# Kernel optimization log

Hardware: AMD Instinct MI355X
Metric: run time of the kernel (lower is better)

The kernel has to match this reference:

```python
import jax, jax.numpy as jnp
import numpy as np

B, M, E, NPOS, F, NHEAD, NLAYERS, DFF = 32, 512, 512, 1024, 768, 8, 2, 2048
S = M + 1

def _pe(embed, pad):
    pos = np.arange(pad, dtype=np.float32)[:, None]
    i = np.arange(embed)[None, :]
    ang = pos / np.power(10000.0, (i // 2 * 2.0) / embed)
    pe = np.where(i % 2 == 0, np.sin(ang), np.cos(ang))
    return jnp.asarray(pe, jnp.float32)

PE = _pe(E, M)  # [M, E] sinusoidal table, matches pos_embedding()

def _ln(x, w, b, eps=1e-5):
    mu = x.mean(-1, keepdims=True)
    var = ((x - mu) ** 2).mean(-1, keepdims=True)
    return (x - mu) / jnp.sqrt(var + eps) * w + b

def _mha(x, wi, bi, wo, bo):
    # x: [L, N, E] where L is the attended axis (torch seq dim)
    L, N, Em = x.shape
    Dh = Em // NHEAD
    q, k, v = jnp.split(x @ wi.T + bi, 3, axis=-1)
    q = q.reshape(L, N, NHEAD, Dh) * np.float32(1.0 / np.sqrt(Dh))
    k = k.reshape(L, N, NHEAD, Dh)
    v = v.reshape(L, N, NHEAD, Dh)
    att = jax.nn.softmax(jnp.einsum('lnhd,mnhd->nhlm', q, k), axis=-1)
    o = jnp.einsum('nhlm,mnhd->lnhd', att, v).reshape(L, N, Em)
    return o @ wo.T + bo

def _encoder(x, enc):
    wi, bi, wo, bo, ln1w, ln1b, ln2w, ln2b, w1, b1, w2, b2 = enc
    for l in range(NLAYERS):  # post-norm TransformerEncoderLayer, ReLU, eval mode
        x = _ln(x + _mha(x, wi[l], bi[l], wo[l], bo[l]), ln1w[l], ln1b[l])
        h = jax.nn.relu(x @ w1[l].T + b1[l]) @ w2[l].T + b2[l]
        x = _ln(x + h, ln2w[l], ln2b[l])
    return x

def _forward(pos1, pos2, bert_feature, final_base, emb_table, enc, w_model, w_disc, b_disc):
    emb_table = emb_table.at[0].set(0.0)  # padding_idx=0
    embed = emb_table[pos2] + PE          # [B, M, E]
    starts, ends = pos1[..., 0], pos1[..., 1]
    # loop breaks at first span with end==0: valid = prefix of nonzero ends
    valid = jnp.cumprod((ends != 0).astype(jnp.int32), axis=1).astype(bool)
    k = jnp.arange(M)
    cover = valid[:, :, None] & (starts[:, :, None] <= k) & (k < ends[:, :, None])  # [B, Mspan, Mpos]
    # later spans overwrite earlier ones -> take max covering span index
    span_id = jnp.max(jnp.where(cover, jnp.arange(M)[None, :, None], -1), axis=1)  # [B, Mpos]
    filled = jnp.take_along_axis(embed, jnp.clip(span_id, 0, M - 1)[..., None], axis=1)
    final = jnp.where(span_id[..., None] >= 0, filled, final_base)  # [B, M, E]
    cls = jnp.broadcast_to(emb_table[1], (B, 1, E))
    x = jnp.concatenate([cls, final], axis=1)  # [B, S, E]; torch encoder treats dim0 as seq
    x = _encoder(x, enc)
    pos_feature = jnp.tanh(x @ w_model.T)      # [B, S, F]
    z = jnp.concatenate([bert_feature, pos_feature], axis=-1) @ w_disc.T + b_disc
    return jax.nn.sigmoid(z)                   # [B, S, 1]

def setup_inputs():
    key = jax.random.key(0)
    ks = jax.random.split(key, 12)
    sc = 0.02
    n_valid, chunk = 120, 4  # contiguous spans [4j, 4j+4) for j < 120, then end==0 terminator
    j = np.arange(M)
    starts = np.where(j < n_valid, j * chunk, 0)
    ends = np.where(j < n_valid, j * chunk + chunk, 0)
    pos1 = np.broadcast_to(np.stack([starts, ends], -1), (B, M, 2)).astype(np.int32)
    return {
        'pos1': jnp.asarray(pos1),
        'pos2': jax.random.randint(ks[0], (B, M), 2, NPOS),
        'bert_feature': jax.random.normal(ks[1], (B, S, F), jnp.float32),
        'final_base': jax.random.uniform(ks[2], (B, M, E), jnp.float32),
        'emb_table': jax.random.normal(ks[3], (NPOS, E), jnp.float32) * sc,
        'enc_in_proj_w': jax.random.normal(ks[4], (NLAYERS, 3 * E, E), jnp.float32) * sc,
        'enc_in_proj_b': jnp.zeros((NLAYERS, 3 * E), jnp.float32),
        'enc_out_proj_w': jax.random.normal(ks[5], (NLAYERS, E, E), jnp.float32) * sc,
        'enc_out_proj_b': jnp.zeros((NLAYERS, E), jnp.float32),
        'enc_ln1_w': jnp.ones((NLAYERS, E), jnp.float32),
        'enc_ln1_b': jnp.zeros((NLAYERS, E), jnp.float32),
        'enc_ln2_w': jnp.ones((NLAYERS, E), jnp.float32),
        'enc_ln2_b': jnp.zeros((NLAYERS, E), jnp.float32),
        'enc_ffn_w1': jax.random.normal(ks[6], (NLAYERS, DFF, E), jnp.float32) * sc,
        'enc_ffn_b1': jnp.zeros((NLAYERS, DFF), jnp.float32),
        'enc_ffn_w2': jax.random.normal(ks[7], (NLAYERS, E, DFF), jnp.float32) * sc,
        'enc_ffn_b2': jnp.zeros((NLAYERS, E), jnp.float32),
        'w_model': jax.random.normal(ks[8], (F, E), jnp.float32) * sc,
        'w_disc': jax.random.normal(ks[9], (1, 2 * F), jnp.float32) * sc,
        'b_disc': jnp.zeros((1,), jnp.float32),
    }

def reference(pos1, pos2, bert_feature, final_base, emb_table,
              enc_in_proj_w, enc_in_proj_b, enc_out_proj_w, enc_out_proj_b,
              enc_ln1_w, enc_ln1_b, enc_ln2_w, enc_ln2_b,
              enc_ffn_w1, enc_ffn_b1, enc_ffn_w2, enc_ffn_b2,
              w_model, w_disc, b_disc):
    enc = (enc_in_proj_w, enc_in_proj_b, enc_out_proj_w, enc_out_proj_b,
           enc_ln1_w, enc_ln1_b, enc_ln2_w, enc_ln2_b,
           enc_ffn_w1, enc_ffn_b1, enc_ffn_w2, enc_ffn_b2)
    return _forward(pos1, pos2, bert_feature, final_base, emb_table, enc, w_model, w_disc, b_disc)
```

## Files before the change

### kernel.cpp

```cpp
#include <hip/hip_runtime.h>
#include <hip/hip_bf16.h>

#define B_   32
#define M_   512
#define E_   512
#define S_   513
#define T_   (B_ * S_)
#define TP_  16512
#define NH_  8
#define DH_  64
#define F_   768
#define DFF_ 2048

#define GMT_ 129

typedef short short8 __attribute__((ext_vector_type(8)));
typedef float floatx4 __attribute__((ext_vector_type(4)));

__device__ __forceinline__ float bf2f(unsigned short u) {
    return __uint_as_float(((unsigned int)u) << 16);
}
__device__ __forceinline__ unsigned short f2b_rne(float f) {
    unsigned int u = __float_as_uint(f);
    unsigned int r = u + 0x7FFF + ((u >> 16) & 1);
    return (unsigned short)(r >> 16);
}
__device__ __forceinline__ void gload16(const void* g, void* l) {
    __builtin_amdgcn_global_load_lds(
        (const __attribute__((address_space(1))) void*)g,
        (__attribute__((address_space(3))) void*)l, 16, 0, 0);
}

__global__ void span_kernel(const int* __restrict__ pos1, int* __restrict__ span) {
    int b = blockIdx.x;
    __shared__ int st[M_], en[M_];
    __shared__ int redm[4];
    int tid = threadIdx.x;
    for (int j = tid; j < M_; j += 256) {
        st[j] = pos1[(b * M_ + j) * 2];
        en[j] = pos1[(b * M_ + j) * 2 + 1];
    }
    __syncthreads();
    int idx = M_;
    for (int j = tid; j < M_; j += 256)
        if (en[j] == 0 && j < idx) idx = j;
    for (int off = 32; off; off >>= 1) idx = min(idx, __shfl_down(idx, off));
    if ((tid & 63) == 0) redm[tid >> 6] = idx;
    __syncthreads();
    int n = min(min(redm[0], redm[1]), min(redm[2], redm[3]));
    for (int k = tid; k < M_; k += 256) {
        int best = -1;
        for (int j = 0; j < n; ++j)
            if (st[j] <= k && k < en[j]) best = j;
        span[b * M_ + k] = best;
    }
}

__global__ void f2b5_kernel(const float* __restrict__ s0, const float* __restrict__ s1,
                            const float* __restrict__ s2, const float* __restrict__ s3,
                            const float* __restrict__ s4,
                            unsigned short* __restrict__ dst,
                            int c0, int c1, int c2, int c3, int c4) {
    int i = (blockIdx.x * 256 + threadIdx.x) * 4;
    if (i >= c4) return;
    const float* src;
    if      (i < c0) src = s0 + i;
    else if (i < c1) src = s1 + (i - c0);
    else if (i < c2) src = s2 + (i - c1);
    else if (i < c3) src = s3 + (i - c2);
    else             src = s4 + (i - c3);
    float4 v = *(const float4*)src;
    ushort4 o;
    o.x = f2b_rne(v.x); o.y = f2b_rne(v.y); o.z = f2b_rne(v.z); o.w = f2b_rne(v.w);
    *(ushort4*)&dst[i] = o;
}

__global__ __launch_bounds__(256) void build_x(const float* __restrict__ emb,
                        const int* __restrict__ pos2,
                        const float* __restrict__ fbase,
                        const int* __restrict__ span,
                        float* __restrict__ x,
                        unsigned short* __restrict__ xb) {
    int gid = blockIdx.x * 256 + threadIdx.x;
    int t  = gid >> 6;
    int e0 = (gid & 63) * 8;
    int s = t % S_;
    int b = t / S_;
    float v[8];
    if (s == 0) {
        float4 a = *(const float4*)&emb[E_ + e0];
        float4 c = *(const float4*)&emb[E_ + e0 + 4];
        v[0]=a.x; v[1]=a.y; v[2]=a.z; v[3]=a.w; v[4]=c.x; v[5]=c.y; v[6]=c.z; v[7]=c.w;
    } else {
        int k = s - 1;
        int sid = span[b * M_ + k];
        if (sid >= 0) {
            int p = pos2[b * M_ + sid];
            const float* er = emb + (size_t)p * E_ + e0;
            float4 a = *(const float4*)er;
            float4 c = *(const float4*)(er + 4);
            v[0]=a.x; v[1]=a.y; v[2]=a.z; v[3]=a.w; v[4]=c.x; v[5]=c.y; v[6]=c.z; v[7]=c.w;
            float fs = (float)sid;
#pragma unroll
            for (int jj = 0; jj < 4; ++jj) {
                float ex = (float)(e0 + 2 * jj) * (1.0f / 512.0f);
                float ang = fs * exp2f(-ex * 13.287712379549449f);
                float sn, cs;
                __sincosf(ang, &sn, &cs);
                v[2 * jj]     += sn;
                v[2 * jj + 1] += cs;
            }
        } else {
            const float* fr = fbase + ((size_t)b * M_ + k) * E_ + e0;
            float4 a = *(const float4*)fr;
            float4 c = *(const float4*)(fr + 4);
            v[0]=a.x; v[1]=a.y; v[2]=a.z; v[3]=a.w; v[4]=c.x; v[5]=c.y; v[6]=c.z; v[7]=c.w;
        }
    }
    size_t o = (size_t)t * E_ + e0;
    *(float4*)&x[o]     = make_float4(v[0], v[1], v[2], v[3]);
    *(float4*)&x[o + 4] = make_float4(v[4], v[5], v[6], v[7]);
    short8 ob;
#pragma unroll
    for (int j = 0; j < 8; ++j) ob[j] = (short)f2b_rne(v[j]);
    *(short8*)&xb[o] = ob;
}

template <int ACT, int KT>
__global__ __launch_bounds__(256, 3) void gemm_bf16(const unsigned short* __restrict__ A,
                                                    const unsigned short* __restrict__ W,
                                                    const float* __restrict__ bias,
                                                    unsigned short* __restrict__ Cb,
                                                    int T, int O,
                                                    const float* __restrict__ wdz,
                                                    float* __restrict__ zout) {
    constexpr int K = KT;
    constexpr int NSTEP = K / 32;
    __shared__ __align__(16) unsigned short sA[3][128 * 32];
    __shared__ __align__(16) unsigned short sB[3][128 * 32];
    int tid = threadIdx.x;
    int lane = tid & 63, wv = tid >> 6;
    int wr = (wv >> 1) * 64, wc = (wv & 1) * 64;

    int gn = O / 128;
    int per_panel = 8 * gn;
    int id = blockIdx.x;
    int p = id / per_panel;
    int r = id - p * per_panel;
    int mrem = GMT_ - p * 8; if (mrem > 8) mrem = 8;
    int mt = p * 8 + r % mrem;
    int nt = r / mrem;
    int t0 = mt * 128, o0 = nt * 128;

    floatx4 acc[4][4] = {};

    int swz_st = (((lane & 3) ^ ((lane >> 3) & 3))) * 8;
    const unsigned short* Ag = A + (size_t)(t0 + wv * 32 + (lane >> 2)) * K + swz_st;
    const unsigned short* Bg = W + (size_t)(o0 + wv * 32 + (lane >> 2)) * K + swz_st;
    const size_t row16 = (size_t)16 * K;
    const int wvo = wv * 1024;

    int fr = lane & 15;
    int fks = (((lane >> 4) ^ ((lane >> 1) & 3))) * 8;

    auto stage = [&](unsigned short* da, unsigned short* db, int k) {
        gload16(Ag + k, da + wvo);
        gload16(Ag + row16 + k, da + wvo + 512);
        gload16(Bg + k, db + wvo);
        gload16(Bg + row16 + k, db + wvo + 512);
    };
    auto compute = [&](const unsigned short* ca, const unsigned short* cb) {
        short8 af[4], bfr[4];
#pragma unroll
        for (int i = 0; i < 4; ++i)
            af[i] = *(const short8*)&ca[(wr + i * 16 + fr) * 32 + fks];
#pragma unroll
        for (int j = 0; j < 4; ++j)
            bfr[j] = *(const short8*)&cb[(wc + j * 16 + fr) * 32 + fks];
        __builtin_amdgcn_s_setprio(1);
#pragma unroll
        for (int i = 0; i < 4; ++i)
#pragma unroll
            for (int j = 0; j < 4; ++j)
                acc[i][j] = __builtin_amdgcn_mfma_f32_16x16x32_bf16(af[i], bfr[j], acc[i][j], 0, 0, 0);
        __builtin_amdgcn_s_setprio(0);
    };

    unsigned short *a0 = sA[0], *a1 = sA[1], *a2 = sA[2];
    unsigned short *b0 = sB[0], *b1 = sB[1], *b2 = sB[2];

    stage(a0, b0, 0);
    stage(a1, b1, 32);

#pragma unroll 3
    for (int t = 0; t < NSTEP - 2; ++t) {
        asm volatile("s_waitcnt vmcnt(4)" ::: "memory");
        __builtin_amdgcn_s_barrier();
        asm volatile("" ::: "memory");
        stage(a2, b2, (t + 2) * 32);
        compute(a0, b0);
        unsigned short* ta = a0; a0 = a1; a1 = a2; a2 = ta;
        unsigned short* tb = b0; b0 = b1; b1 = b2; b2 = tb;
    }
    asm volatile("s_waitcnt vmcnt(4)" ::: "memory");
    __builtin_amdgcn_s_barrier();
    asm volatile("" ::: "memory");
    compute(a0, b0);
    a0 = a1; b0 = b1;
    asm volatile("s_waitcnt vmcnt(0)" ::: "memory");
    __builtin_amdgcn_s_barrier();
    asm volatile("" ::: "memory");
    compute(a0, b0);

    int cr = (lane >> 4) * 4;
    int cc = lane & 15;
    if (ACT == 2) {
        float zp[4][4];
#pragma unroll
        for (int i = 0; i < 4; ++i)
#pragma unroll
            for (int rr = 0; rr < 4; ++rr) zp[i][rr] = 0.f;
#pragma unroll
        for (int j = 0; j < 4; ++j) {
            int gn_ = o0 + wc + j * 16 + cc;
            float wz = wdz[gn_];
#pragma unroll
            for (int i = 0; i < 4; ++i)
#pragma unroll
                for (int rr = 0; rr < 4; ++rr)
                    zp[i][rr] += tanhf(acc[i][j][rr]) * wz;
        }
#pragma unroll
        for (int i = 0; i < 4; ++i)
#pragma unroll
            for (int rr = 0; rr < 4; ++rr) {
                float v = zp[i][rr];
                v += __shfl_xor(v, 1);
                v += __shfl_xor(v, 2);
                v += __shfl_xor(v, 4);
                v += __shfl_xor(v, 8);
                if (cc == 0) {
                    int gm_ = t0 + wr + i * 16 + cr + rr;
                    if (gm_ < T) atomicAdd(&zout[gm_], v);
                }
            }
        return;
    }
#pragma unroll
    for (int i = 0; i < 4; ++i) {
#pragma unroll
        for (int j = 0; j < 4; ++j) {
            int gn_ = o0 + wc + j * 16 + cc;
            float bv = bias ? bias[gn_] : 0.f;
#pragma unroll
            for (int rr = 0; rr < 4; ++rr) {
                int gm_ = t0 + wr + i * 16 + cr + rr;
                if (gm_ >= T) continue;
                float v = acc[i][j][rr] + bv;
                if (ACT == 1) v = fmaxf(v, 0.f);
                Cb[(size_t)gm_ * O + gn_] = f2b_rne(v);
            }
        }
    }
}

__global__ __launch_bounds__(64) void attn_mfma(const unsigned short* __restrict__ qkv,
                                                unsigned short* __restrict__ o) {
    __shared__ __align__(16) unsigned short vt[64 * 40];
    __shared__ __align__(16) unsigned short ps[32 * 40];
    int s = blockIdx.x, h = blockIdx.y;
    int lane = threadIdx.x;
    int hd = h * 64;
    int fr = lane & 15, fq = lane >> 4;

    {
        int m = lane >> 1;
        int d0 = (lane & 1) * 32;
        const unsigned short* vrow = qkv + ((size_t)m * S_ + s) * 1536 + 1024 + hd + d0;
        short8 v0 = *(const short8*)(vrow);
        short8 v1 = *(const short8*)(vrow + 8);
        short8 v2 = *(const short8*)(vrow + 16);
        short8 v3 = *(const short8*)(vrow + 24);
#pragma unroll
        for (int j = 0; j < 8; ++j) {
            vt[(d0 + j) * 40 + m]      = (unsigned short)v0[j];
            vt[(d0 + 8 + j) * 40 + m]  = (unsigned short)v1[j];
            vt[(d0 + 16 + j) * 40 + m] = (unsigned short)v2[j];
            vt[(d0 + 24 + j) * 40 + m] = (unsigned short)v3[j];
        }
    }

    floatx4 c[2][2] = {};
#pragma unroll
    for (int ks = 0; ks < 2; ++ks) {
        short8 aq[2], bk[2];
#pragma unroll
        for (int lt = 0; lt < 2; ++lt) {
            int l = lt * 16 + fr;
            aq[lt] = *(const short8*)(qkv + ((size_t)l * S_ + s) * 1536 + hd + ks * 32 + fq * 8);
        }
#pragma unroll
        for (int mt = 0; mt < 2; ++mt) {
            int m = mt * 16 + fr;
            bk[mt] = *(const short8*)(qkv + ((size_t)m * S_ + s) * 1536 + 512 + hd + ks * 32 + fq * 8);
        }
#pragma unroll
        for (int lt = 0; lt < 2; ++lt)
#pragma unroll
            for (int mt = 0; mt < 2; ++mt)
                c[lt][mt] = __builtin_amdgcn_mfma_f32_16x16x32_bf16(aq[lt], bk[mt], c[lt][mt], 0, 0, 0);
    }

#pragma unroll
    for (int lt = 0; lt < 2; ++lt) {
#pragma unroll
        for (int r = 0; r < 4; ++r) {
            float a = c[lt][0][r] * 0.125f;
            float b = c[lt][1][r] * 0.125f;
            float mx = fmaxf(a, b);
#pragma unroll
            for (int off = 1; off < 16; off <<= 1) mx = fmaxf(mx, __shfl_xor(mx, off));
            float ea = expf(a - mx), eb = expf(b - mx);
            float sm = ea + eb;
#pragma unroll
            for (int off = 1; off < 16; off <<= 1) sm += __shfl_xor(sm, off);
            float inv = 1.f / sm;
            int l = lt * 16 + fq * 4 + r;
            ps[l * 40 + fr]      = f2b_rne(ea * inv);
            ps[l * 40 + 16 + fr] = f2b_rne(eb * inv);
        }
    }
    __syncthreads();

    short8 pa[2], vb[4];
#pragma unroll
    for (int lt = 0; lt < 2; ++lt)
        pa[lt] = *(const short8*)&ps[(lt * 16 + fr) * 40 + fq * 8];
#pragma unroll
    for (int dt = 0; dt < 4; ++dt)
        vb[dt] = *(const short8*)&vt[(dt * 16 + fr) * 40 + fq * 8];

    floatx4 oa[2][4] = {};
#pragma unroll
    for (int lt = 0; lt < 2; ++lt)
#pragma unroll
        for (int dt = 0; dt < 4; ++dt)
            oa[lt][dt] = __builtin_amdgcn_mfma_f32_16x16x32_bf16(pa[lt], vb[dt], oa[lt][dt], 0, 0, 0);

#pragma unroll
    for (int lt = 0; lt < 2; ++lt)
#pragma unroll
        for (int dt = 0; dt < 4; ++dt)
#pragma unroll
            for (int r = 0; r < 4; ++r) {
                int l = lt * 16 + fq * 4 + r;
                o[((size_t)l * S_ + s) * E_ + hd + dt * 16 + fr] = f2b_rne(oa[lt][dt][r]);
            }
}

__global__ __launch_bounds__(256) void add_ln(float* __restrict__ x,
                                              unsigned short* __restrict__ xb,
                                              const unsigned short* __restrict__ h,
                                              const float* __restrict__ w,
                                              const float* __restrict__ b) {
    int t = (blockIdx.x << 2) + (threadIdx.x >> 6);
    int lane = threadIdx.x & 63;
    int i0 = lane * 8;
    float* xr = x + (size_t)t * E_;
    const unsigned short* hr = h + (size_t)t * E_;
    float4 xv0 = *(const float4*)&xr[i0];
    float4 xv1 = *(const float4*)&xr[i0 + 4];
    short8 hv = *(const short8*)&hr[i0];
    float v[8];
    v[0] = xv0.x + bf2f((unsigned short)hv[0]);
    v[1] = xv0.y + bf2f((unsigned short)hv[1]);
    v[2] = xv0.z + bf2f((unsigned short)hv[2]);
    v[3] = xv0.w + bf2f((unsigned short)hv[3]);
    v[4] = xv1.x + bf2f((unsigned short)hv[4]);
    v[5] = xv1.y + bf2f((unsigned short)hv[5]);
    v[6] = xv1.z + bf2f((unsigned short)hv[6]);
    v[7] = xv1.w + bf2f((unsigned short)hv[7]);

    float sum = 0.f;
#pragma unroll
    for (int j = 0; j < 8; ++j) sum += v[j];
#pragma unroll
    for (int off = 32; off; off >>= 1) sum += __shfl_xor(sum, off);
    float mu = sum * (1.0f / E_);

    float qs = 0.f;
#pragma unroll
    for (int j = 0; j < 8; ++j) { float d = v[j] - mu; qs += d * d; }
#pragma unroll
    for (int off = 32; off; off >>= 1) qs += __shfl_xor(qs, off);
    float rstd = rsqrtf(qs * (1.0f / E_) + 1e-5f);

    float4 wv0 = *(const float4*)&w[i0];
    float4 wv1 = *(const float4*)&w[i0 + 4];
    float4 bv0 = *(const float4*)&b[i0];
    float4 bv1 = *(const float4*)&b[i0 + 4];
    float o[8];
    o[0] = (v[0] - mu) * rstd * wv0.x + bv0.x;
    o[1] = (v[1] - mu) * rstd * wv0.y + bv0.y;
    o[2] = (v[2] - mu) * rstd * wv0.z + bv0.z;
    o[3] = (v[3] - mu) * rstd * wv0.w + bv0.w;
    o[4] = (v[4] - mu) * rstd * wv1.x + bv1.x;
    o[5] = (v[5] - mu) * rstd * wv1.y + bv1.y;
    o[6] = (v[6] - mu) * rstd * wv1.z + bv1.z;
    o[7] = (v[7] - mu) * rstd * wv1.w + bv1.w;
    *(float4*)&xr[i0]     = make_float4(o[0], o[1], o[2], o[3]);
    *(float4*)&xr[i0 + 4] = make_float4(o[4], o[5], o[6], o[7]);
    short8 ob;
#pragma unroll
    for (int j = 0; j < 8; ++j) ob[j] = (short)f2b_rne(o[j]);
    *(short8*)&xb[(size_t)t * E_ + i0] = ob;
}

__global__ __launch_bounds__(256) void disc_kernel(const float* __restrict__ bert,
                                                   const float* __restrict__ z,
                                                   const float* __restrict__ wd,
                                                   const float* __restrict__ bd,
                                                   float* __restrict__ out) {
    int t = (blockIdx.x << 2) + (threadIdx.x >> 6);
    int lane = threadIdx.x & 63;
    int i0 = lane * 12;
    const float* br = bert + (size_t)t * F_ + i0;
    const float* wr = wd + i0;
    float s = 0.f;
#pragma unroll
    for (int j = 0; j < 12; j += 4) {
        float4 bv = *(const float4*)(br + j);
        float4 wv = *(const float4*)(wr + j);
        s += bv.x * wv.x + bv.y * wv.y + bv.z * wv.z + bv.w * wv.w;
    }
#pragma unroll
    for (int off = 32; off; off >>= 1) s += __shfl_xor(s, off);
    if (lane == 0) {
        float zz = s + z[t] + bd[0];
        out[t] = 1.f / (1.f + expf(-zz));
    }
}

extern "C" void kernel_launch(void* const* d_in, const int* in_sizes, int n_in,
                              void* d_out, int out_size, void* d_ws, size_t ws_size,
                              hipStream_t stream) {
    const int*   pos1 = (const int*)d_in[0];
    const int*   pos2 = (const int*)d_in[1];
    const float* bert = (const float*)d_in[2];
    const float* fb   = (const float*)d_in[3];
    const float* emb  = (const float*)d_in[4];
    const float* wi   = (const float*)d_in[5];
    const float* bi   = (const float*)d_in[6];
    const float* wo   = (const float*)d_in[7];
    const float* bo   = (const float*)d_in[8];
    const float* ln1w = (const float*)d_in[9];
    const float* ln1b = (const float*)d_in[10];
    const float* ln2w = (const float*)d_in[11];
    const float* ln2b = (const float*)d_in[12];
    const float* w1   = (const float*)d_in[13];
    const float* b1   = (const float*)d_in[14];
    const float* w2   = (const float*)d_in[15];
    const float* b2   = (const float*)d_in[16];
    const float* wm   = (const float*)d_in[17];
    const float* wd   = (const float*)d_in[18];
    const float* bd   = (const float*)d_in[19];
    float* out = (float*)d_out;

    float* ws   = (float*)d_ws;
    int*   span = (int*)ws;
    float* x    = ws + 16384;
    unsigned short* xb  = (unsigned short*)(x + (size_t)T_ * 512);
    unsigned short* atb = xb + (size_t)TP_ * 512;
    unsigned short* hb  = atb + (size_t)TP_ * 512;
    unsigned short* U   = hb + (size_t)T_ * 512;
    unsigned short* qkvb = U;
    unsigned short* h1b  = U;
    unsigned short* wib  = U + (size_t)TP_ * 2048;
    const int NWI = 2 * 1536 * 512;
    const int NWO = 2 * 512 * 512;
    const int NW1 = 2 * 2048 * 512;
    const int NW2 = 2 * 512 * 2048;
    const int NWM = 768 * 512;
    unsigned short* wob = wib + NWI;
    unsigned short* w1b = wob + NWO;
    unsigned short* w2b = w1b + NW1;
    unsigned short* wmb = w2b + NW2;
    float* z = (float*)atb;

    span_kernel<<<B_, 256, 0, stream>>>(pos1, span);
    {
        int c0 = NWI, c1 = c0 + NWO, c2 = c1 + NW1, c3 = c2 + NW2, c4 = c3 + NWM;
        f2b5_kernel<<<(c4 / 4 + 255) / 256, 256, 0, stream>>>(wi, wo, w1, w2, wm, wib,
                                                              c0, c1, c2, c3, c4);
    }
    build_x<<<T_ / 4, 256, 0, stream>>>(emb, pos2, fb, span, x, xb);

    for (int l = 0; l < 2; ++l) {
        gemm_bf16<0, 512><<<GMT_ * (1536 / 128), 256, 0, stream>>>(
            xb, wib + (size_t)l * 1536 * 512, bi + l * 1536, qkvb, T_, 1536, nullptr, nullptr);
        attn_mfma<<<dim3(S_, NH_), 64, 0, stream>>>(qkvb, atb);
        gemm_bf16<0, 512><<<GMT_ * (512 / 128), 256, 0, stream>>>(
            atb, wob + (size_t)l * 512 * 512, bo + l * 512, hb, T_, 512, nullptr, nullptr);
        add_ln<<<T_ / 4, 256, 0, stream>>>(x, xb, hb, ln1w + l * 512, ln1b + l * 512);
        gemm_bf16<1, 512><<<GMT_ * (2048 / 128), 256, 0, stream>>>(
            xb, w1b + (size_t)l * 2048 * 512, b1 + l * 2048, h1b, T_, 2048, nullptr, nullptr);
        gemm_bf16<0, 2048><<<GMT_ * (512 / 128), 256, 0, stream>>>(
            h1b, w2b + (size_t)l * 512 * 2048, b2 + l * 512, hb, T_, 512, nullptr, nullptr);
        add_ln<<<T_ / 4, 256, 0, stream>>>(x, xb, hb, ln2w + l * 512, ln2b + l * 512);
    }
    hipMemsetAsync(z, 0, (size_t)T_ * sizeof(float), stream);
    gemm_bf16<2, 512><<<GMT_ * (768 / 128), 256, 0, stream>>>(
        xb, wmb, nullptr, nullptr, T_, 768, wd + F_, z);
    disc_kernel<<<T_ / 4, 256, 0, stream>>>(bert, z, wd, bd, out);
}
```

Baseline: 732.9 us.

## Load GEMM A operand directly from global into registers, skip final fp32 x write

The GEMM kernel no longer stages the A tile through shared memory. Each wave loads its A fragments straight from global memory into registers, while only the weight tile goes through a triple-buffered LDS pipeline. This halves LDS use, which allows four blocks per CU instead of three. The A loads are no longer shared between the two waves that need the same rows, so global and L2 traffic rises and load latency is exposed inside the loop. Separately, the last layer's LayerNorm skips writing the fp32 residual, since only the bf16 copy is read afterwards.

```diff
diff --git a/kernel.cpp b/kernel.cpp
--- a/kernel.cpp
+++ b/kernel.cpp
@@ -127,7 +127,7 @@
 }
 
 template <int ACT, int KT>
-__global__ __launch_bounds__(256, 3) void gemm_bf16(const unsigned short* __restrict__ A,
+__global__ __launch_bounds__(256, 4) void gemm_bf16(const unsigned short* __restrict__ A,
                                                     const unsigned short* __restrict__ W,
                                                     const float* __restrict__ bias,
                                                     unsigned short* __restrict__ Cb,
@@ -136,7 +136,6 @@
                                                     float* __restrict__ zout) {
     constexpr int K = KT;
     constexpr int NSTEP = K / 32;
-    __shared__ __align__(16) unsigned short sA[3][128 * 32];
     __shared__ __align__(16) unsigned short sB[3][128 * 32];
     int tid = threadIdx.x;
     int lane = tid & 63, wv = tid >> 6;
@@ -154,29 +153,42 @@
 
     floatx4 acc[4][4] = {};
 
+    int fr = lane & 15;
+    int fq = lane >> 4;
+
+    const unsigned short* Af = A + (size_t)(t0 + wr + fr) * K + fq * 8;
+
     int swz_st = (((lane & 3) ^ ((lane >> 3) & 3))) * 8;
-    const unsigned short* Ag = A + (size_t)(t0 + wv * 32 + (lane >> 2)) * K + swz_st;
     const unsigned short* Bg = W + (size_t)(o0 + wv * 32 + (lane >> 2)) * K + swz_st;
     const size_t row16 = (size_t)16 * K;
     const int wvo = wv * 1024;
-
-    int fr = lane & 15;
-    int fks = (((lane >> 4) ^ ((lane >> 1) & 3))) * 8;
-
-    auto stage = [&](unsigned short* da, unsigned short* db, int k) {
-        gload16(Ag + k, da + wvo);
-        gload16(Ag + row16 + k, da + wvo + 512);
+    int fks = ((fq ^ ((lane >> 1) & 3))) * 8;
+
+    auto stage = [&](unsigned short* db, int k) {
         gload16(Bg + k, db + wvo);
         gload16(Bg + row16 + k, db + wvo + 512);
     };
-    auto compute = [&](const unsigned short* ca, const unsigned short* cb) {
-        short8 af[4], bfr[4];
-#pragma unroll
-        for (int i = 0; i < 4; ++i)
-            af[i] = *(const short8*)&ca[(wr + i * 16 + fr) * 32 + fks];
+
+    unsigned short *b0 = sB[0], *b1 = sB[1], *b2 = sB[2];
+
+    stage(b0, 0);
+    stage(b1, 32);
+
+#pragma unroll 2
+    for (int t = 0; t < NSTEP - 2; ++t) {
+        asm volatile("s_waitcnt vmcnt(2)" ::: "memory");
+        __builtin_amdgcn_s_barrier();
+        asm volatile("" ::: "memory");
+        short8 af[4];
+#pragma unroll
+        for (int i = 0; i < 4; ++i)
+            af[i] = *(const short8*)(Af + (size_t)i * 16 * K + t * 32);
+        __builtin_amdgcn_sched_barrier(0);
+        stage(b2, (t + 2) * 32);
+        short8 bfr[4];
 #pragma unroll
         for (int j = 0; j < 4; ++j)
-            bfr[j] = *(const short8*)&cb[(wc + j * 16 + fr) * 32 + fks];
+            bfr[j] = *(const short8*)&b0[(wc + j * 16 + fr) * 32 + fks];
         __builtin_amdgcn_s_setprio(1);
 #pragma unroll
         for (int i = 0; i < 4; ++i)
@@ -184,36 +196,45 @@
             for (int j = 0; j < 4; ++j)
                 acc[i][j] = __builtin_amdgcn_mfma_f32_16x16x32_bf16(af[i], bfr[j], acc[i][j], 0, 0, 0);
         __builtin_amdgcn_s_setprio(0);
-    };
-
-    unsigned short *a0 = sA[0], *a1 = sA[1], *a2 = sA[2];
-    unsigned short *b0 = sB[0], *b1 = sB[1], *b2 = sB[2];
-
-    stage(a0, b0, 0);
-    stage(a1, b1, 32);
-
-#pragma unroll 3
-    for (int t = 0; t < NSTEP - 2; ++t) {
-        asm volatile("s_waitcnt vmcnt(4)" ::: "memory");
-        __builtin_amdgcn_s_barrier();
-        asm volatile("" ::: "memory");
-        stage(a2, b2, (t + 2) * 32);
-        compute(a0, b0);
-        unsigned short* ta = a0; a0 = a1; a1 = a2; a2 = ta;
         unsigned short* tb = b0; b0 = b1; b1 = b2; b2 = tb;
     }
-    asm volatile("s_waitcnt vmcnt(4)" ::: "memory");
+    asm volatile("s_waitcnt vmcnt(2)" ::: "memory");
     __builtin_amdgcn_s_barrier();
     asm volatile("" ::: "memory");
-    compute(a0, b0);
-    a0 = a1; b0 = b1;
+    {
+        short8 af[4], bfr[4];
+#pragma unroll
+        for (int i = 0; i < 4; ++i)
+            af[i] = *(const short8*)(Af + (size_t)i * 16 * K + (NSTEP - 2) * 32);
+#pragma unroll
+        for (int j = 0; j < 4; ++j)
+            bfr[j] = *(const short8*)&b0[(wc + j * 16 + fr) * 32 + fks];
+#pragma unroll
+        for (int i = 0; i < 4; ++i)
+#pragma unroll
+            for (int j = 0; j < 4; ++j)
+                acc[i][j] = __builtin_amdgcn_mfma_f32_16x16x32_bf16(af[i], bfr[j], acc[i][j], 0, 0, 0);
+    }
     asm volatile("s_waitcnt vmcnt(0)" ::: "memory");
     __builtin_amdgcn_s_barrier();
     asm volatile("" ::: "memory");
-    compute(a0, b0);
-
-    int cr = (lane >> 4) * 4;
-    int cc = lane & 15;
+    {
+        short8 af[4], bfr[4];
+#pragma unroll
+        for (int i = 0; i < 4; ++i)
+            af[i] = *(const short8*)(Af + (size_t)i * 16 * K + (NSTEP - 1) * 32);
+#pragma unroll
+        for (int j = 0; j < 4; ++j)
+            bfr[j] = *(const short8*)&b1[(wc + j * 16 + fr) * 32 + fks];
+#pragma unroll
+        for (int i = 0; i < 4; ++i)
+#pragma unroll
+            for (int j = 0; j < 4; ++j)
+                acc[i][j] = __builtin_amdgcn_mfma_f32_16x16x32_bf16(af[i], bfr[j], acc[i][j], 0, 0, 0);
+    }
+
+    int cr = fq * 4;
+    int cc = fr;
     if (ACT == 2) {
         float zp[4][4];
 #pragma unroll
@@ -358,6 +379,7 @@
             }
 }
 
+template <bool WX>
 __global__ __launch_bounds__(256) void add_ln(float* __restrict__ x,
                                               unsigned short* __restrict__ xb,
                                               const unsigned short* __restrict__ h,
@@ -408,8 +430,10 @@
     o[5] = (v[5] - mu) * rstd * wv1.y + bv1.y;
     o[6] = (v[6] - mu) * rstd * wv1.z + bv1.z;
     o[7] = (v[7] - mu) * rstd * wv1.w + bv1.w;
-    *(float4*)&xr[i0]     = make_float4(o[0], o[1], o[2], o[3]);
-    *(float4*)&xr[i0 + 4] = make_float4(o[4], o[5], o[6], o[7]);
+    if (WX) {
+        *(float4*)&xr[i0]     = make_float4(o[0], o[1], o[2], o[3]);
+        *(float4*)&xr[i0 + 4] = make_float4(o[4], o[5], o[6], o[7]);
+    }
     short8 ob;
 #pragma unroll
     for (int j = 0; j < 8; ++j) ob[j] = (short)f2b_rne(o[j]);
@@ -501,12 +525,15 @@
         attn_mfma<<<dim3(S_, NH_), 64, 0, stream>>>(qkvb, atb);
         gemm_bf16<0, 512><<<GMT_ * (512 / 128), 256, 0, stream>>>(
             atb, wob + (size_t)l * 512 * 512, bo + l * 512, hb, T_, 512, nullptr, nullptr);
-        add_ln<<<T_ / 4, 256, 0, stream>>>(x, xb, hb, ln1w + l * 512, ln1b + l * 512);
+        add_ln<true><<<T_ / 4, 256, 0, stream>>>(x, xb, hb, ln1w + l * 512, ln1b + l * 512);
         gemm_bf16<1, 512><<<GMT_ * (2048 / 128), 256, 0, stream>>>(
             xb, w1b + (size_t)l * 2048 * 512, b1 + l * 2048, h1b, T_, 2048, nullptr, nullptr);
         gemm_bf16<0, 2048><<<GMT_ * (512 / 128), 256, 0, stream>>>(
             h1b, w2b + (size_t)l * 512 * 2048, b2 + l * 512, hb, T_, 512, nullptr, nullptr);
-        add_ln<<<T_ / 4, 256, 0, stream>>>(x, xb, hb, ln2w + l * 512, ln2b + l * 512);
+        if (l == 0)
+            add_ln<true><<<T_ / 4, 256, 0, stream>>>(x, xb, hb, ln2w + l * 512, ln2b + l * 512);
+        else
+            add_ln<false><<<T_ / 4, 256, 0, stream>>>(x, xb, hb, ln2w + l * 512, ln2b + l * 512);
     }
     hipMemsetAsync(z, 0, (size_t)T_ * sizeof(float), stream);
     gemm_bf16<2, 512><<<GMT_ * (768 / 128), 256, 0, stream>>>(
```

Result: slower. 1.000 ms (+36.5%).
